# Optimization experiments

Hardware: AMD Instinct MI355X
Metric: run time of the kernel (lower is better)

The kernel has to match this reference:

```python
import jax, jax.numpy as jnp
import numpy as np

B, T, C = 2, 2048, 2048
H = 16
D = C // H  # 128 head dim
EPS = 1.1920929e-07  # torch RMSNorm default eps for fp32 (finfo.eps)
ROPE_BASE = 1000000.0


def setup_inputs() -> dict:
    key = jax.random.key(0)
    k1, k2, k3 = jax.random.split(key, 3)
    x = jax.random.normal(k1, (B, T, C), dtype=jnp.float32)
    w_qkv = jax.random.normal(k2, (C, 3 * C), dtype=jnp.float32) * (C ** -0.5)
    w_proj = jax.random.normal(k3, (C, C), dtype=jnp.float32) * (C ** -0.5)
    q_norm_w = jnp.ones((D,), dtype=jnp.float32)
    k_norm_w = jnp.ones((D,), dtype=jnp.float32)
    return {"x": x, "w_qkv": w_qkv, "w_proj": w_proj,
            "q_norm_w": q_norm_w, "k_norm_w": k_norm_w}


def _rms_norm(x, w):
    var = jnp.mean(jnp.square(x), axis=-1, keepdims=True)
    return x * jax.lax.rsqrt(var + EPS) * w


def _rope_tables(t_len, d_head, dtype):
    inv_freq = 1.0 / (ROPE_BASE ** (jnp.arange(0, d_head, 2, dtype=jnp.float32) / d_head))
    t = jnp.arange(t_len, dtype=jnp.float32)
    freqs = jnp.einsum('i,j->ij', t, inv_freq)          # [T, D/2]
    emb = jnp.concatenate([freqs, freqs], axis=-1)      # [T, D]
    return jnp.cos(emb).astype(dtype), jnp.sin(emb).astype(dtype)


def _rotate_half(x):
    x1, x2 = x[..., : x.shape[-1] // 2], x[..., x.shape[-1] // 2:]
    return jnp.concatenate([-x2, x1], axis=-1)


def reference(x, w_qkv, w_proj, q_norm_w, k_norm_w):
    b, t, c = x.shape
    qkv = x @ w_qkv                                     # [B, T, 3C]
    q, k, v = jnp.split(qkv, 3, axis=-1)
    # [B, H, T, D]
    q = q.reshape(b, t, H, D).transpose(0, 2, 1, 3)
    k = k.reshape(b, t, H, D).transpose(0, 2, 1, 3)
    v = v.reshape(b, t, H, D).transpose(0, 2, 1, 3)
    q = _rms_norm(q, q_norm_w)
    k = _rms_norm(k, k_norm_w)
    cos, sin = _rope_tables(t, D, x.dtype)              # [T, D]
    q = q * cos + _rotate_half(q) * sin
    k = k * cos + _rotate_half(k) * sin
    # NOTE: module uses scale = 1/d_head, not 1/sqrt(d_head)
    scale = 1.0 / D
    att = jnp.einsum('bhqd,bhkd->bhqk', q, k) * scale   # [B, H, T, T]
    causal = jnp.tril(jnp.ones((t, t), dtype=bool))
    att = jnp.where(causal, att, jnp.finfo(att.dtype).min)
    att = jax.nn.softmax(att, axis=-1)
    y = jnp.einsum('bhqk,bhkd->bhqd', att, v)           # [B, H, T, D]
    y = y.transpose(0, 2, 1, 3).reshape(b, t, c)
    return y @ w_proj
```

## Files before the change

### kernel.cpp

```cpp
#include <hip/hip_runtime.h>
#include <stdint.h>

#define Bb   2
#define Tt   2048
#define Cc_  2048
#define Hh   16
#define Dd   128
#define Mm_  4096
#define N1   6144
#define EPSf 1.1920929e-07f
#define SCALE (1.0f/128.0f)

typedef __bf16 bf16;
typedef __attribute__((ext_vector_type(8))) __bf16 bf16x8;
typedef __attribute__((ext_vector_type(4))) __bf16 bf16x4;
typedef __attribute__((ext_vector_type(4))) float  f32x4;

__device__ __forceinline__ void gl_lds16(const bf16* g, bf16* l) {
  __builtin_amdgcn_global_load_lds(
      (const __attribute__((address_space(1))) unsigned int*)g,
      (__attribute__((address_space(3))) unsigned int*)l, 16, 0, 0);
}

__global__ __launch_bounds__(256) void cvt_bf16(const float* __restrict__ in,
                                                bf16* __restrict__ out, int n) {
  int i = (blockIdx.x * 256 + threadIdx.x) * 4;
  if (i >= n) return;
  float4 v = *(const float4*)(in + i);
  union { bf16 h[4]; uint2 u; } o;
  o.h[0] = (bf16)v.x; o.h[1] = (bf16)v.y; o.h[2] = (bf16)v.z; o.h[3] = (bf16)v.w;
  *(uint2*)(out + i) = o.u;
}

__global__ __launch_bounds__(256) void rope_tab(float2* __restrict__ rope) {
  int i = blockIdx.x * 256 + threadIdx.x;
  int t = i >> 6, d = i & 63;
  float ang = (float)t * exp2f((float)d * (-19.9315685693241740f / 64.0f));
  float sn, cs;
  sincosf(ang, &sn, &cs);
  rope[i] = make_float2(cs, sn);
}

__global__ __launch_bounds__(256) void transpose_cvt(const float* __restrict__ in,
                                                     bf16* __restrict__ out,
                                                     int R, int Cc) {
  __shared__ float tile[64][65];
  int c0 = blockIdx.x * 64, r0 = blockIdx.y * 64;
  int tid = threadIdx.x;
#pragma unroll
  for (int j = 0; j < 16; ++j) {
    int idx = tid + j * 256;
    int r = idx >> 6, c = idx & 63;
    tile[r][c] = in[(size_t)(r0 + r) * Cc + c0 + c];
  }
  __syncthreads();
#pragma unroll
  for (int j = 0; j < 16; ++j) {
    int idx = tid + j * 256;
    int rr = idx & 63, cc = idx >> 6;
    out[(size_t)(c0 + cc) * R + r0 + rr] = (bf16)tile[rr][cc];
  }
}

__global__ __launch_bounds__(256) void gemm_qkv_fused(
    const bf16* __restrict__ A, const bf16* __restrict__ Bt,
    const float* __restrict__ qw, const float* __restrict__ kw,
    const float2* __restrict__ rope,
    bf16* __restrict__ Qg, bf16* __restrict__ Kg, bf16* __restrict__ VgT) {
  __shared__ __align__(16) bf16 smem[128 * 136];
  bf16* As = smem;
  bf16* Bs = smem + 128 * 64;
  const int Kk = Cc_;
  const int tid = threadIdx.x;
  const int wave = tid >> 6, lane = tid & 63;
  const int quad = lane >> 4, li = lane & 15;
  const int wm = wave >> 1, wn = wave & 1;
  const int m0 = blockIdx.y * 128, n0 = blockIdx.x * 128;

  f32x4 acc[4][4] = {};

  for (int kt = 0; kt < Kk; kt += 64) {
    __syncthreads();
#pragma unroll
    for (int j = 0; j < 4; ++j) {
      int c = j * 256 + tid;
      int r = c >> 3, cc = c & 7;
      int gc = ((cc ^ (r & 7)) << 3);
      gl_lds16(A + (size_t)(m0 + r) * Kk + kt + gc, &As[c * 8]);
      gl_lds16(Bt + (size_t)(n0 + r) * Kk + kt + gc, &Bs[c * 8]);
    }
    __syncthreads();
#pragma unroll
    for (int kc = 0; kc < 2; ++kc) {
      bf16x8 af[4], bfr[4];
#pragma unroll
      for (int t = 0; t < 4; ++t) {
        int rowa = wm * 64 + t * 16 + li;
        af[t] = *(const bf16x8*)&As[rowa * 64 + (((kc * 4 + quad) ^ (rowa & 7)) << 3)];
        int rowb = wn * 64 + t * 16 + li;
        bfr[t] = *(const bf16x8*)&Bs[rowb * 64 + (((kc * 4 + quad) ^ (rowb & 7)) << 3)];
      }
#pragma unroll
      for (int mi = 0; mi < 4; ++mi)
#pragma unroll
        for (int ni = 0; ni < 4; ++ni)
          acc[mi][ni] = __builtin_amdgcn_mfma_f32_16x16x32_bf16(af[mi], bfr[ni],
                                                                acc[mi][ni], 0, 0, 0);
    }
  }

  __syncthreads();
  const int s = blockIdx.x;
  const int b = m0 >> 11;
  const int tloc = m0 & 2047;
  bf16 (*tile)[136] = (bf16(*)[136])smem;

  if (s < 32) {
#pragma unroll
    for (int mi = 0; mi < 4; ++mi) {
      int row = wm * 64 + mi * 16 + quad * 4;
#pragma unroll
      for (int ni = 0; ni < 4; ++ni) {
        int col = wn * 64 + ni * 16 + li;
#pragma unroll
        for (int r = 0; r < 4; ++r)
          tile[row + r][col] = (bf16)acc[mi][ni][r];
      }
    }
    __syncthreads();

    const float* w = (s < 16) ? qw : kw;
    bf16* Og = (s < 16) ? Qg : Kg;
    const int h = s & 15;
    const size_t hb = (size_t)(b * Hh + h) * Tt;
    float w1[4], w2[4];
#pragma unroll
    for (int j = 0; j < 4; ++j) { w1[j] = w[li * 4 + j]; w2[j] = w[64 + li * 4 + j]; }
#pragma unroll
    for (int it = 0; it < 8; ++it) {
      int row = wave * 32 + it * 4 + quad;
      int t = tloc + row;
      bf16x4 x1 = *(const bf16x4*)&tile[row][li * 4];
      bf16x4 x2 = *(const bf16x4*)&tile[row][64 + li * 4];
      float f1[4], f2[4];
      float ss = 0.f;
#pragma unroll
      for (int j = 0; j < 4; ++j) {
        f1[j] = (float)x1[j]; f2[j] = (float)x2[j];
        ss += f1[j] * f1[j] + f2[j] * f2[j];
      }
#pragma unroll
      for (int o = 1; o < 16; o <<= 1) ss += __shfl_xor(ss, o);
      float rn = rsqrtf(ss * (1.0f / 128.0f) + EPSf);
      const float4* rp = (const float4*)(rope + t * 64 + li * 4);
      float4 ra = rp[0], rb = rp[1];
      float cs[4] = {ra.x, ra.z, rb.x, rb.z};
      float sn[4] = {ra.y, ra.w, rb.y, rb.w};
      bf16x4 o1, o2;
#pragma unroll
      for (int j = 0; j < 4; ++j) {
        float a1 = f1[j] * rn * w1[j], a2 = f2[j] * rn * w2[j];
        o1[j] = (bf16)(a1 * cs[j] - a2 * sn[j]);
        o2[j] = (bf16)(a2 * cs[j] + a1 * sn[j]);
      }
      size_t ob = (hb + t) * Dd + li * 4;
      *(bf16x4*)(Og + ob)      = o1;
      *(bf16x4*)(Og + ob + 64) = o2;
    }
  } else {
#pragma unroll
    for (int mi = 0; mi < 4; ++mi) {
      int row = wm * 64 + mi * 16 + quad * 4;
#pragma unroll
      for (int ni = 0; ni < 4; ++ni) {
        int col = wn * 64 + ni * 16 + li;
#pragma unroll
        for (int r = 0; r < 4; ++r)
          tile[col][row + r] = (bf16)acc[mi][ni][r];
      }
    }
    __syncthreads();
    const int h = s - 32;
    const size_t hb = (size_t)(b * Hh + h) * Dd;
#pragma unroll
    for (int it = 0; it < 8; ++it) {
      int d  = it * 16 + (tid >> 4);
      int t0 = (tid & 15) * 8;
      bf16x8 v = *(const bf16x8*)&tile[d][t0];
      *(bf16x8*)(VgT + (hb + d) * Tt + tloc + t0) = v;
    }
  }
}

template <typename OutT>
__global__ __launch_bounds__(512, 2) void gemm256(const bf16* __restrict__ A,
                                                  const bf16* __restrict__ Bt,
                                                  OutT* __restrict__ Cm,
                                                  int Nn, int Kk) {
  __shared__ __align__(16) bf16 As[2][256 * 64];
  __shared__ __align__(16) bf16 Bs[2][128 * 64];
  const int tid = threadIdx.x;
  const int wave = tid >> 6, lane = tid & 63;
  const int quad = lane >> 4, li = lane & 15;
  const int wm = wave >> 2, wn = wave & 3;

  const int nwg = gridDim.x * gridDim.y;
  const int wg  = blockIdx.y * gridDim.x + blockIdx.x;
  const int swz = (wg & 7) * (nwg >> 3) + (wg >> 3);
  const int m0 = (swz / gridDim.x) * 256;
  const int n0 = (swz % gridDim.x) * 128;

  const int NT = Kk >> 6;
  const int lrow = lane >> 3;
  const int lchk = (lane & 7) ^ lrow;

  auto stageA = [&](int tt, int h, int cb) {
    int kt = (tt < NT ? tt : NT - 1) << 6;
#pragma unroll
    for (int j = 0; j < 2; ++j) {
      int seg = j * 8 + wave;
      int r0 = ((seg >> 3) << 7) + (h << 6) + ((seg & 7) << 3);
      gl_lds16(A + (size_t)(m0 + r0 + lrow) * Kk + kt + (lchk << 3),
               &As[cb][r0 * 64]);
    }
  };
  auto stageB = [&](int tt, int cb) {
    int kt = (tt < NT ? tt : NT - 1) << 6;
#pragma unroll
    for (int j = 0; j < 2; ++j) {
      int seg = j * 8 + wave;
      int r0 = seg << 3;
      gl_lds16(Bt + (size_t)(n0 + r0 + lrow) * Kk + kt + (lchk << 3),
               &Bs[cb][r0 * 64]);
    }
  };

  f32x4 acc[8][2] = {};
  bf16x8 afr[4][2], bfr[2][2];

  auto rdA = [&](int h, int cb) {
#pragma unroll
    for (int mi = 0; mi < 4; ++mi) {
      int r = wm * 128 + h * 64 + mi * 16 + li;
#pragma unroll
      for (int kc = 0; kc < 2; ++kc)
        afr[mi][kc] = *(const bf16x8*)&As[cb][r * 64 + (((kc * 4 + quad) ^ (r & 7)) << 3)];
    }
  };
  auto rdB = [&](int cb) {
#pragma unroll
    for (int nj = 0; nj < 2; ++nj) {
      int r = wn * 32 + nj * 16 + li;
#pragma unroll
      for (int kc = 0; kc < 2; ++kc)
        bfr[nj][kc] = *(const bf16x8*)&Bs[cb][r * 64 + (((kc * 4 + quad) ^ (r & 7)) << 3)];
    }
  };
  auto mmac = [&](int mo) {
    __builtin_amdgcn_s_setprio(1);
#pragma unroll
    for (int kc = 0; kc < 2; ++kc)
#pragma unroll
      for (int mi = 0; mi < 4; ++mi)
#pragma unroll
        for (int nj = 0; nj < 2; ++nj)
          acc[mo + mi][nj] = __builtin_amdgcn_mfma_f32_16x16x32_bf16(
              afr[mi][kc], bfr[nj][kc], acc[mo + mi][nj], 0, 0, 0);
    __builtin_amdgcn_s_setprio(0);
  };

  auto tile = [&](int t, int cur, int nxt) {
    rdA(0, cur); rdB(cur);
    stageA(t + 1, 1, nxt);
    asm volatile("s_waitcnt lgkmcnt(8)" ::: "memory");
    __builtin_amdgcn_s_barrier();
    asm volatile("s_waitcnt lgkmcnt(0)" ::: "memory");
    __builtin_amdgcn_sched_barrier(0);
    mmac(0);
    asm volatile("s_waitcnt vmcnt(6)" ::: "memory");
    __builtin_amdgcn_s_barrier();
    rdA(1, cur);
    stageA(t + 2, 0, cur);
    stageB(t + 2, cur);
    __builtin_amdgcn_s_barrier();
    asm volatile("s_waitcnt lgkmcnt(0)" ::: "memory");
    __builtin_amdgcn_sched_barrier(0);
    mmac(4);
    asm volatile("s_waitcnt vmcnt(6)" ::: "memory");
    __builtin_amdgcn_s_barrier();
  };

  stageA(0, 0, 0); stageB(0, 0); stageA(0, 1, 0);
  stageA(1, 0, 1); stageB(1, 1);
  asm volatile("s_waitcnt vmcnt(6)" ::: "memory");
  __builtin_amdgcn_s_barrier();

  for (int t = 0; t < NT; t += 2) {
    tile(t, 0, 1);
    tile(t + 1, 1, 0);
  }
  asm volatile("s_waitcnt vmcnt(0)" ::: "memory");

#pragma unroll
  for (int mi = 0; mi < 8; ++mi) {
    int row = m0 + wm * 128 + mi * 16 + quad * 4;
#pragma unroll
    for (int nj = 0; nj < 2; ++nj) {
      int col = n0 + wn * 32 + nj * 16 + li;
#pragma unroll
      for (int r = 0; r < 4; ++r)
        Cm[(size_t)(row + r) * Nn + col] = (OutT)acc[mi][nj][r];
    }
  }
}

__global__ __launch_bounds__(256, 3) void attn(const bf16* __restrict__ Qg,
                                               const bf16* __restrict__ Kg,
                                               const bf16* __restrict__ VgT,
                                               bf16* __restrict__ Yg) {
  __shared__ __align__(16) bf16 Kl[64 * 128];
  __shared__ __align__(16) bf16 Vl[128 * 64];
  __shared__ __align__(16) bf16 Pl[4 * 16 * 72];
  const int bh = blockIdx.x;
  const int qt = (int)gridDim.y - 1 - (int)blockIdx.y;
  const int b = bh >> 4, h = bh & 15;
  const int tid = threadIdx.x, wave = tid >> 6, lane = tid & 63;
  const int quad = lane >> 4, li = lane & 15;
  const int q0 = qt * 64;

  const bf16* Qbase = Qg + ((size_t)bh * Tt + q0 + wave * 16 + li) * Dd;
  bf16x8 qf[4];
#pragma unroll
  for (int kc = 0; kc < 4; ++kc) qf[kc] = *(const bf16x8*)(Qbase + kc * 32 + quad * 8);

  f32x4 o[8] = {};
  float L[4] = {};
  bf16* Pw = &Pl[wave * 16 * 72];

  bf16x8 kreg[4];
  auto loadK = [&](int k0) {
#pragma unroll
    for (int j = 0; j < 4; ++j) {
      int c = j * 256 + tid;
      int r = c >> 4, cc = c & 15;
      kreg[j] = *(const bf16x8*)(Kg + ((size_t)bh * Tt + k0 + r) * Dd + ((cc ^ (r & 7)) << 3));
    }
  };
  auto stageV = [&](int k0) {
#pragma unroll
    for (int j = 0; j < 4; ++j) {
      int c = j * 256 + tid;
      int r = c >> 3, cc = c & 7;
      gl_lds16(VgT + ((size_t)bh * Dd + r) * Tt + k0 + ((cc ^ (r & 7)) << 3), &Vl[c * 8]);
    }
  };

  loadK(0);
  stageV(0);

  for (int kt = 0; kt <= qt; ++kt) {
    asm volatile("s_waitcnt vmcnt(4)" ::: "memory");
#pragma unroll
    for (int j = 0; j < 4; ++j) {
      int c = j * 256 + tid;
      *(bf16x8*)&Kl[c * 8] = kreg[j];
    }
    if (kt < qt) loadK(kt * 64 + 64);
    asm volatile("s_waitcnt lgkmcnt(0)" ::: "memory");
    __builtin_amdgcn_s_barrier();
    __builtin_amdgcn_sched_barrier(0);

    f32x4 s4[4] = {};
#pragma unroll
    for (int nt = 0; nt < 4; ++nt) {
      int key = nt * 16 + li;
#pragma unroll
      for (int kc = 0; kc < 4; ++kc) {
        bf16x8 kf = *(const bf16x8*)&Kl[key * 128 + (((kc * 4 + quad) ^ (key & 7)) << 3)];
        s4[nt] = __builtin_amdgcn_mfma_f32_16x16x32_bf16(qf[kc], kf, s4[nt], 0, 0, 0);
      }
    }
    const bool diag = (kt == qt);
#pragma unroll
    for (int nt = 0; nt < 4; ++nt)
#pragma unroll
      for (int r = 0; r < 4; ++r) {
        float e = __expf(s4[nt][r] * SCALE);
        if (diag && (nt * 16 + li > wave * 16 + quad * 4 + r)) e = 0.f;
        L[r] += e;
        Pw[(quad * 4 + r) * 72 + nt * 16 + li] = (bf16)e;
      }
    if (kt < qt) { asm volatile("s_waitcnt vmcnt(4)" ::: "memory"); }
    else         { asm volatile("s_waitcnt vmcnt(0)" ::: "memory"); }
    __builtin_amdgcn_s_barrier();
    __builtin_amdgcn_sched_barrier(0);

#pragma unroll
    for (int kc = 0; kc < 2; ++kc) {
      bf16x8 pf = *(const bf16x8*)&Pw[li * 72 + kc * 32 + quad * 8];
#pragma unroll
      for (int u = 0; u < 8; ++u) {
        bf16x8 vf = *(const bf16x8*)&Vl[(u * 16 + li) * 64 + (((kc * 4 + quad) ^ (li & 7)) << 3)];
        o[u] = __builtin_amdgcn_mfma_f32_16x16x32_bf16(pf, vf, o[u], 0, 0, 0);
      }
    }
    asm volatile("" ::: "memory");
    __builtin_amdgcn_s_barrier();
    __builtin_amdgcn_sched_barrier(0);
    if (kt < qt) stageV(kt * 64 + 64);
  }

  float inv[4];
#pragma unroll
  for (int r = 0; r < 4; ++r) {
    float s0 = L[r];
#pragma unroll
    for (int off = 1; off < 16; off <<= 1) s0 += __shfl_xor(s0, off);
    inv[r] = 1.0f / s0;
  }
  int trow = q0 + wave * 16 + quad * 4;
#pragma unroll
  for (int u = 0; u < 8; ++u) {
    int col = h * Dd + u * 16 + li;
#pragma unroll
    for (int r = 0; r < 4; ++r)
      Yg[(size_t)(b * Tt + trow + r) * Cc_ + col] = (bf16)(o[u][r] * inv[r]);
  }
}

extern "C" void kernel_launch(void* const* d_in, const int* in_sizes, int n_in,
                              void* d_out, int out_size, void* d_ws, size_t ws_size,
                              hipStream_t stream) {
  const float* x      = (const float*)d_in[0];
  const float* w_qkv  = (const float*)d_in[1];
  const float* w_proj = (const float*)d_in[2];
  const float* qnw    = (const float*)d_in[3];
  const float* knw    = (const float*)d_in[4];
  float* out = (float*)d_out;

  bf16* xb     = (bf16*)d_ws;
  bf16* wqkvT  = xb + (size_t)Mm_ * Cc_;
  bf16* wprojT = wqkvT + (size_t)N1 * Cc_;
  bf16* Qg     = wprojT + (size_t)Cc_ * Cc_;
  bf16* Kg     = Qg + (size_t)Bb * Hh * Tt * Dd;
  bf16* VgT    = Kg + (size_t)Bb * Hh * Tt * Dd;
  float2* rope = (float2*)(VgT + (size_t)Bb * Hh * Tt * Dd);
  bf16* Yg     = xb;

  hipLaunchKernelGGL(rope_tab, dim3(Tt * 64 / 256), dim3(256), 0, stream, rope);
  hipLaunchKernelGGL(cvt_bf16, dim3((Mm_ * Cc_ / 4) / 256), dim3(256), 0, stream,
                     x, xb, Mm_ * Cc_);
  hipLaunchKernelGGL(transpose_cvt, dim3(N1 / 64, Cc_ / 64), dim3(256), 0, stream,
                     w_qkv, wqkvT, Cc_, N1);
  hipLaunchKernelGGL(transpose_cvt, dim3(Cc_ / 64, Cc_ / 64), dim3(256), 0, stream,
                     w_proj, wprojT, Cc_, Cc_);
  hipLaunchKernelGGL(gemm_qkv_fused, dim3(N1 / 128, Mm_ / 128), dim3(256), 0, stream,
                     xb, wqkvT, qnw, knw, rope, Qg, Kg, VgT);
  hipLaunchKernelGGL(attn, dim3(Bb * Hh, Tt / 64), dim3(256), 0, stream,
                     Qg, Kg, VgT, Yg);
  hipLaunchKernelGGL(gemm256<float>, dim3(Cc_ / 128, Mm_ / 256), dim3(512), 0, stream,
                     Yg, wprojT, out, Cc_, Cc_);
}
```

Baseline: 377.8 us.

## Keep attention P in registers via transposed QK MFMA and lane shuffles

The QK^T MFMA operands are swapped so each lane holds scores for one query row across keys. The softmax numerators are then packed and redistributed with cross-lane shuffles into the PV A-operand, which removes the LDS round-trip through the P buffer. Row-sum reduction is simplified to match the new layout. The change also adds s_setprio around the MFMA blocks, raises the attention occupancy hint to 4 blocks, and vectorizes the transpose kernel's global loads to float4. The risks are the shuffle overhead and register pressure under the tighter launch bound.

```diff
diff --git a/kernel.cpp b/kernel.cpp
--- a/kernel.cpp
+++ b/kernel.cpp
@@ -48,10 +48,11 @@
   int c0 = blockIdx.x * 64, r0 = blockIdx.y * 64;
   int tid = threadIdx.x;
 #pragma unroll
-  for (int j = 0; j < 16; ++j) {
-    int idx = tid + j * 256;
+  for (int j = 0; j < 4; ++j) {
+    int idx = (j * 256 + tid) * 4;
     int r = idx >> 6, c = idx & 63;
-    tile[r][c] = in[(size_t)(r0 + r) * Cc + c0 + c];
+    float4 v = *(const float4*)(in + (size_t)(r0 + r) * Cc + c0 + c);
+    tile[r][c] = v.x; tile[r][c + 1] = v.y; tile[r][c + 2] = v.z; tile[r][c + 3] = v.w;
   }
   __syncthreads();
 #pragma unroll
@@ -314,13 +315,12 @@
   }
 }
 
-__global__ __launch_bounds__(256, 3) void attn(const bf16* __restrict__ Qg,
+__global__ __launch_bounds__(256, 4) void attn(const bf16* __restrict__ Qg,
                                                const bf16* __restrict__ Kg,
                                                const bf16* __restrict__ VgT,
                                                bf16* __restrict__ Yg) {
   __shared__ __align__(16) bf16 Kl[64 * 128];
   __shared__ __align__(16) bf16 Vl[128 * 64];
-  __shared__ __align__(16) bf16 Pl[4 * 16 * 72];
   const int bh = blockIdx.x;
   const int qt = (int)gridDim.y - 1 - (int)blockIdx.y;
   const int b = bh >> 4, h = bh & 15;
@@ -334,8 +334,10 @@
   for (int kc = 0; kc < 4; ++kc) qf[kc] = *(const bf16x8*)(Qbase + kc * 32 + quad * 8);
 
   f32x4 o[8] = {};
-  float L[4] = {};
-  bf16* Pw = &Pl[wave * 16 * 72];
+  float Lq = 0.f;
+  const int s0lane = ((quad & 1) << 5) + li;
+  const int s1lane = s0lane + 16;
+  const bool hi = (quad >> 1) != 0;
 
   bf16x8 kreg[4];
   auto loadK = [&](int k0) {
@@ -371,53 +373,76 @@
     __builtin_amdgcn_sched_barrier(0);
 
     f32x4 s4[4] = {};
+    __builtin_amdgcn_s_setprio(1);
 #pragma unroll
     for (int nt = 0; nt < 4; ++nt) {
       int key = nt * 16 + li;
 #pragma unroll
       for (int kc = 0; kc < 4; ++kc) {
         bf16x8 kf = *(const bf16x8*)&Kl[key * 128 + (((kc * 4 + quad) ^ (key & 7)) << 3)];
-        s4[nt] = __builtin_amdgcn_mfma_f32_16x16x32_bf16(qf[kc], kf, s4[nt], 0, 0, 0);
-      }
-    }
+        s4[nt] = __builtin_amdgcn_mfma_f32_16x16x32_bf16(kf, qf[kc], s4[nt], 0, 0, 0);
+      }
+    }
+    __builtin_amdgcn_s_setprio(0);
+
     const bool diag = (kt == qt);
-#pragma unroll
-    for (int nt = 0; nt < 4; ++nt)
+    uint32_t pk[4][2];
+#pragma unroll
+    for (int nt = 0; nt < 4; ++nt) {
+      float e[4];
 #pragma unroll
       for (int r = 0; r < 4; ++r) {
-        float e = __expf(s4[nt][r] * SCALE);
-        if (diag && (nt * 16 + li > wave * 16 + quad * 4 + r)) e = 0.f;
-        L[r] += e;
-        Pw[(quad * 4 + r) * 72 + nt * 16 + li] = (bf16)e;
-      }
+        e[r] = __expf(s4[nt][r] * SCALE);
+        if (diag && (nt * 16 + quad * 4 + r > wave * 16 + li)) e[r] = 0.f;
+        Lq += e[r];
+      }
+      union { bf16 hh[2]; uint32_t u; } c0_, c1_;
+      c0_.hh[0] = (bf16)e[0]; c0_.hh[1] = (bf16)e[1]; pk[nt][0] = c0_.u;
+      c1_.hh[0] = (bf16)e[2]; c1_.hh[1] = (bf16)e[3]; pk[nt][1] = c1_.u;
+    }
+    bf16x8 pf[2];
+#pragma unroll
+    for (int kc = 0; kc < 2; ++kc) {
+      union { uint32_t u[4]; bf16x8 v; } pu;
+      uint32_t a, bsel;
+      a = __shfl(pk[2 * kc][0], s0lane); bsel = __shfl(pk[2 * kc + 1][0], s0lane);
+      pu.u[0] = hi ? bsel : a;
+      a = __shfl(pk[2 * kc][1], s0lane); bsel = __shfl(pk[2 * kc + 1][1], s0lane);
+      pu.u[1] = hi ? bsel : a;
+      a = __shfl(pk[2 * kc][0], s1lane); bsel = __shfl(pk[2 * kc + 1][0], s1lane);
+      pu.u[2] = hi ? bsel : a;
+      a = __shfl(pk[2 * kc][1], s1lane); bsel = __shfl(pk[2 * kc + 1][1], s1lane);
+      pu.u[3] = hi ? bsel : a;
+      pf[kc] = pu.v;
+    }
+
     if (kt < qt) { asm volatile("s_waitcnt vmcnt(4)" ::: "memory"); }
     else         { asm volatile("s_waitcnt vmcnt(0)" ::: "memory"); }
     __builtin_amdgcn_s_barrier();
     __builtin_amdgcn_sched_barrier(0);
 
+    __builtin_amdgcn_s_setprio(1);
 #pragma unroll
     for (int kc = 0; kc < 2; ++kc) {
-      bf16x8 pf = *(const bf16x8*)&Pw[li * 72 + kc * 32 + quad * 8];
 #pragma unroll
       for (int u = 0; u < 8; ++u) {
         bf16x8 vf = *(const bf16x8*)&Vl[(u * 16 + li) * 64 + (((kc * 4 + quad) ^ (li & 7)) << 3)];
-        o[u] = __builtin_amdgcn_mfma_f32_16x16x32_bf16(pf, vf, o[u], 0, 0, 0);
-      }
-    }
+        o[u] = __builtin_amdgcn_mfma_f32_16x16x32_bf16(pf[kc], vf, o[u], 0, 0, 0);
+      }
+    }
+    __builtin_amdgcn_s_setprio(0);
     asm volatile("" ::: "memory");
     __builtin_amdgcn_s_barrier();
     __builtin_amdgcn_sched_barrier(0);
     if (kt < qt) stageV(kt * 64 + 64);
   }
 
+  Lq += __shfl_xor(Lq, 16);
+  Lq += __shfl_xor(Lq, 32);
+  float invq = 1.0f / Lq;
   float inv[4];
 #pragma unroll
-  for (int r = 0; r < 4; ++r) {
-    float s0 = L[r];
-#pragma unroll
-    for (int off = 1; off < 16; off <<= 1) s0 += __shfl_xor(s0, off);
-    inv[r] = 1.0f / s0;
-  }
+  for (int r = 0; r < 4; ++r) inv[r] = __shfl(invq, quad * 4 + r);
   int trow = q0 + wave * 16 + quad * 4;
 #pragma unroll
   for (int u = 0; u < 8; ++u) {
```

Measured after the change: 392.3 us. 3.9% more time.
